# Kernel tuning notes

Measured on AMD Instinct MI355X. Metric: run time of the kernel, lower is better.

The kernel has to match this reference:

```python
import jax, jax.numpy as jnp
import numpy as np

T = 2048
HIDDEN = 4096
NH = 32        # query heads
NKV = 8        # kv heads
G = NH // NKV  # GQA group size
D = 128        # head_dim (== v_head_dim)
ROPE_BASE = 1000000.0


def setup_inputs() -> dict:
    key = jax.random.key(0)
    ks = jax.random.split(key, 8)
    s = 0.02
    return {
        "positions": jnp.arange(T, dtype=jnp.int32),
        "hidden_states": jax.random.normal(ks[0], (T, HIDDEN), dtype=jnp.float32),
        "Wq": jax.random.normal(ks[1], (HIDDEN, NH * D), dtype=jnp.float32) * s,
        "bq": jnp.zeros((NH * D,), dtype=jnp.float32),
        "Wk": jax.random.normal(ks[2], (HIDDEN, NKV * D), dtype=jnp.float32) * s,
        "bk": jnp.zeros((NKV * D,), dtype=jnp.float32),
        "Wv": jax.random.normal(ks[3], (HIDDEN, NKV * D), dtype=jnp.float32) * s,
        "bv": jnp.zeros((NKV * D,), dtype=jnp.float32),
        "Wo": jax.random.normal(ks[4], (NH * D, HIDDEN), dtype=jnp.float32) * s,
    }


def _rope(positions, x):
    # neox-style rotary, full rotary_dim = D
    half = D // 2
    inv_freq = 1.0 / (ROPE_BASE ** (jnp.arange(0, half, dtype=jnp.float32) / half))
    freqs = positions.astype(jnp.float32)[:, None] * inv_freq[None, :]  # [T, half]
    cos = jnp.cos(freqs)[:, None, :]  # [T, 1, half]
    sin = jnp.sin(freqs)[:, None, :]
    x1, x2 = x[..., :half], x[..., half:]
    return jnp.concatenate([x1 * cos - x2 * sin, x2 * cos + x1 * sin], axis=-1)


def reference(positions, hidden_states, Wq, bq, Wk, bk, Wv, bv, Wo):
    q = (hidden_states @ Wq + bq).reshape(T, NH, D)
    k = (hidden_states @ Wk + bk).reshape(T, NKV, D)
    v = (hidden_states @ Wv + bv).reshape(T, NKV, D)
    q = _rope(positions, q)
    k = _rope(positions, k)

    scale = D ** -0.5
    qg = q.reshape(T, NKV, G, D)
    # scores: [NKV, G, T(query), S(key)]
    scores = jnp.einsum("tkgd,skd->kgts", qg, k) * scale
    causal = positions[:, None] >= positions[None, :]  # [T, S]
    scores = jnp.where(causal[None, None, :, :], scores, jnp.finfo(scores.dtype).min)
    probs = jax.nn.softmax(scores, axis=-1)
    attn = jnp.einsum("kgts,skd->tkgd", probs, v).reshape(T, NH * D)

    output = attn @ Wo
    kv_fused = jnp.stack([k, v], axis=0)  # [2, T, NKV, D]
    return output, kv_fused
```

## Files before the change

### kernel.cpp

```cpp
#include <hip/hip_runtime.h>
#include <stdint.h>

#define T_SEQ 2048
#define HIDDEN_DIM 4096
#define NH 32
#define NKV 8
#define HD 128
#define QKV_N 6144

typedef unsigned short u16;
typedef __attribute__((__ext_vector_type__(8))) __bf16 bf16x8;
typedef __attribute__((__ext_vector_type__(4))) float f32x4;

__device__ __forceinline__ u16 f2bf(float f) {
    union { float f; unsigned u; } x; x.f = f;
    unsigned u = x.u;
    unsigned r = u + 0x7FFFu + ((u >> 16) & 1u);
    return (u16)(r >> 16);
}
__device__ __forceinline__ float bf2f(u16 h) {
    union { unsigned u; float f; } x; x.u = ((unsigned)h) << 16;
    return x.f;
}

__device__ __forceinline__ void gl_lds16(const u16* g, u16* l) {
    __builtin_amdgcn_global_load_lds((__attribute__((address_space(1))) void*)g,
                                     (__attribute__((address_space(3))) void*)l,
                                     16, 0, 0);
}

__global__ __launch_bounds__(256) void cast_f32_bf16(const float* __restrict__ in,
                                                     u16* __restrict__ out, int n4) {
    int i = blockIdx.x * 256 + threadIdx.x;
    if (i < n4) {
        float4 v = ((const float4*)in)[i];
        uint2 o;
        o.x = (unsigned)f2bf(v.x) | ((unsigned)f2bf(v.y) << 16);
        o.y = (unsigned)f2bf(v.z) | ((unsigned)f2bf(v.w) << 16);
        ((uint2*)out)[i] = o;
    }
}

__global__ __launch_bounds__(256) void transpose_cast(const float* __restrict__ W,
                                                      u16* __restrict__ Wt, int R, int C) {
    __shared__ float tile[32][33];
    int c0 = blockIdx.x * 32, r0 = blockIdx.y * 32;
    int tx = threadIdx.x & 31;
    int ty = threadIdx.x >> 5;
#pragma unroll
    for (int i = 0; i < 32; i += 8)
        tile[ty + i][tx] = W[(size_t)(r0 + ty + i) * C + c0 + tx];
    __syncthreads();
#pragma unroll
    for (int i = 0; i < 32; i += 8)
        Wt[(size_t)(c0 + ty + i) * R + r0 + tx] = f2bf(tile[tx][ty + i]);
}

__global__ __launch_bounds__(256) void concat_bias(const float* __restrict__ bq,
                                                   const float* __restrict__ bk,
                                                   const float* __restrict__ bv,
                                                   float* __restrict__ out) {
    int i = blockIdx.x * 256 + threadIdx.x;
    if (i < 4096) out[i] = bq[i];
    else if (i < 5120) out[i] = bk[i - 4096];
    else if (i < 6144) out[i] = bv[i - 5120];
}

template <int BF16_OUT, int HAS_BIAS>
__global__ __launch_bounds__(256) void gemm_bt(const u16* __restrict__ A,
                                               const u16* __restrict__ Bt,
                                               const float* __restrict__ bias,
                                               void* __restrict__ Cv,
                                               int M, int N, int K) {
    __shared__ alignas(16) u16 As[128 * 32];
    __shared__ alignas(16) u16 Bs[128 * 32];
    const int tid = threadIdx.x;
    const int wave = tid >> 6;
    const int lane = tid & 63;
    const int l15 = lane & 15;
    const int quad = lane >> 4;
    const int m0 = blockIdx.y * 128;
    const int n0 = blockIdx.x * 128;
    const int wm = (wave >> 1) * 64;
    const int wn = (wave & 1) * 64;

    f32x4 acc[4][4] = {};

    const u16* Ag = A + (size_t)(m0 + wave * 32 + (lane >> 2)) * K + (lane & 3) * 8;
    const u16* Bg = Bt + (size_t)(n0 + wave * 32 + (lane >> 2)) * K + (lane & 3) * 8;
    u16* Al = &As[wave * 32 * 32];
    u16* Bl = &Bs[wave * 32 * 32];

    for (int k0 = 0; k0 < K; k0 += 32) {
        __syncthreads();
        gl_lds16(Ag + k0, Al);
        gl_lds16(Ag + k0 + (size_t)16 * K, Al + 16 * 32);
        gl_lds16(Bg + k0, Bl);
        gl_lds16(Bg + k0 + (size_t)16 * K, Bl + 16 * 32);
        __syncthreads();
        bf16x8 af[4], bfr[4];
#pragma unroll
        for (int i = 0; i < 4; ++i)
            af[i] = *(const bf16x8*)&As[(wm + i * 16 + l15) * 32 + quad * 8];
#pragma unroll
        for (int i = 0; i < 4; ++i)
            bfr[i] = *(const bf16x8*)&Bs[(wn + i * 16 + l15) * 32 + quad * 8];
#pragma unroll
        for (int i = 0; i < 4; ++i)
#pragma unroll
            for (int j = 0; j < 4; ++j)
                acc[i][j] = __builtin_amdgcn_mfma_f32_16x16x32_bf16(af[i], bfr[j], acc[i][j], 0, 0, 0);
    }

#pragma unroll
    for (int i = 0; i < 4; ++i)
#pragma unroll
        for (int j = 0; j < 4; ++j)
#pragma unroll
            for (int r = 0; r < 4; ++r) {
                int row = m0 + wm + i * 16 + quad * 4 + r;
                int col = n0 + wn + j * 16 + l15;
                float v = acc[i][j][r];
                if (HAS_BIAS) v += bias[col];
                if (BF16_OUT) ((u16*)Cv)[(size_t)row * N + col] = f2bf(v);
                else ((float*)Cv)[(size_t)row * N + col] = v;
            }
}

__global__ __launch_bounds__(256) void rope_kernel(const int* __restrict__ positions,
                                                   const u16* __restrict__ qkv,
                                                   u16* __restrict__ qh,
                                                   u16* __restrict__ kh,
                                                   u16* __restrict__ vt,
                                                   float* __restrict__ kv_out) {
    const int t = blockIdx.x;
    const float pos = (float)positions[t];
    const size_t rowbase = (size_t)t * QKV_N;
    const float nlog = -13.815510557964274f / 64.f;
    for (int col = threadIdx.x; col < QKV_N; col += 256) {
        if (col < 4096) {
            int hh = col >> 7, d = col & 127, j = d & 63;
            float ang = pos * __expf((float)j * nlog);
            float cs = cosf(ang), sn = sinf(ang);
            size_t base = rowbase + (size_t)(col & ~127);
            float x1 = bf2f(qkv[base + j]);
            float x2 = bf2f(qkv[base + 64 + j]);
            float v = (d < 64) ? (x1 * cs - x2 * sn) : (x2 * cs + x1 * sn);
            qh[((size_t)hh * T_SEQ + t) * HD + d] = f2bf(v);
        } else if (col < 5120) {
            int lc = col - 4096, hh = lc >> 7, d = lc & 127, j = d & 63;
            float ang = pos * __expf((float)j * nlog);
            float cs = cosf(ang), sn = sinf(ang);
            size_t base = rowbase + 4096 + (size_t)hh * 128;
            float x1 = bf2f(qkv[base + j]);
            float x2 = bf2f(qkv[base + 64 + j]);
            float v = (d < 64) ? (x1 * cs - x2 * sn) : (x2 * cs + x1 * sn);
            kh[((size_t)hh * T_SEQ + t) * HD + d] = f2bf(v);
            kv_out[((size_t)t * NKV + hh) * HD + d] = v;
        } else {
            int lc = col - 5120, hh = lc >> 7, d = lc & 127;
            float v = bf2f(qkv[rowbase + 5120 + (size_t)hh * 128 + d]);
            vt[((size_t)hh * HD + d) * T_SEQ + t] = f2bf(v);
            kv_out[(((size_t)T_SEQ + t) * NKV + hh) * HD + d] = v;
        }
    }
}

#define KS_STRIDE 136
#define VS_STRIDE 72
#define PS_STRIDE 72

__global__ __launch_bounds__(256) void attn_kernel(const u16* __restrict__ Qh,
                                                   const u16* __restrict__ Kh,
                                                   const u16* __restrict__ Vt,
                                                   u16* __restrict__ attn_out) {
    __shared__ alignas(16) u16 Ks[64 * KS_STRIDE];
    __shared__ alignas(16) u16 Vs[128 * VS_STRIDE];
    __shared__ alignas(16) u16 Ps[4][32 * PS_STRIDE];

    const int h = blockIdx.y;
    const int qb = (gridDim.x - 1) - blockIdx.x;
    const int tid = threadIdx.x;
    const int wave = tid >> 6;
    const int lane = tid & 63;
    const int l15 = lane & 15;
    const int quad = lane >> 4;
    const int kvh = h >> 2;
    const int wrow0 = qb * 128 + wave * 32;

    const u16* Qp = Qh + ((size_t)h * T_SEQ + wrow0) * HD;
    const u16* Kp = Kh + (size_t)kvh * T_SEQ * HD;
    const u16* Vp = Vt + (size_t)kvh * HD * T_SEQ;

    bf16x8 aQ[2][4];
#pragma unroll
    for (int i = 0; i < 2; ++i)
#pragma unroll
        for (int kb = 0; kb < 4; ++kb)
            aQ[i][kb] = *(const bf16x8*)&Qp[(size_t)(i * 16 + l15) * HD + kb * 32 + quad * 8];

    f32x4 acc[2][8] = {};
    float mrow[2][4], lrow[2][4];
#pragma unroll
    for (int i = 0; i < 2; ++i)
#pragma unroll
        for (int r = 0; r < 4; ++r) { mrow[i][r] = -1e30f; lrow[i][r] = 0.f; }

    const float scale = 0.08838834764831845f;
    const int s_hi = qb * 128 + 128;

    const int krow = tid >> 4;
    const int kcol = (tid & 15) * 8;
    const int vrow = tid >> 3;
    const int vcol = (tid & 7) * 8;

    for (int s0 = 0; s0 < s_hi; s0 += 64) {
        __syncthreads();
#pragma unroll
        for (int rep = 0; rep < 4; ++rep) {
            int r = krow + rep * 16;
            *(uint4*)&Ks[r * KS_STRIDE + kcol] =
                *(const uint4*)&Kp[(size_t)(s0 + r) * HD + kcol];
        }
#pragma unroll
        for (int rep = 0; rep < 4; ++rep) {
            int d = vrow + rep * 32;
            *(uint4*)&Vs[d * VS_STRIDE + vcol] =
                *(const uint4*)&Vp[(size_t)d * T_SEQ + s0 + vcol];
        }
        __syncthreads();

        if (s0 <= wrow0 + 31) {
            f32x4 sc[2][4];
#pragma unroll
            for (int j = 0; j < 4; ++j) {
                f32x4 sa = {}, sb = {};
#pragma unroll
                for (int kb = 0; kb < 4; ++kb) {
                    bf16x8 bK = *(const bf16x8*)&Ks[(j * 16 + l15) * KS_STRIDE + kb * 32 + quad * 8];
                    sa = __builtin_amdgcn_mfma_f32_16x16x32_bf16(aQ[0][kb], bK, sa, 0, 0, 0);
                    sb = __builtin_amdgcn_mfma_f32_16x16x32_bf16(aQ[1][kb], bK, sb, 0, 0, 0);
                }
                sc[0][j] = sa;
                sc[1][j] = sb;
            }
#pragma unroll
            for (int i = 0; i < 2; ++i)
#pragma unroll
                for (int r = 0; r < 4; ++r) {
                    int t_idx = wrow0 + i * 16 + quad * 4 + r;
                    float pv[4];
                    float vmax = -1e30f;
#pragma unroll
                    for (int j = 0; j < 4; ++j) {
                        int s_idx = s0 + j * 16 + l15;
                        float v = sc[i][j][r] * scale;
                        v = (s_idx > t_idx) ? -1e30f : v;
                        pv[j] = v;
                        vmax = fmaxf(vmax, v);
                    }
#pragma unroll
                    for (int off = 1; off < 16; off <<= 1)
                        vmax = fmaxf(vmax, __shfl_xor(vmax, off));
                    float mn = fmaxf(mrow[i][r], vmax);
                    float alpha = __expf(mrow[i][r] - mn);
                    mrow[i][r] = mn;
                    float rs = 0.f;
#pragma unroll
                    for (int j = 0; j < 4; ++j) {
                        pv[j] = __expf(pv[j] - mn);
                        rs += pv[j];
                    }
#pragma unroll
                    for (int off = 1; off < 16; off <<= 1)
                        rs += __shfl_xor(rs, off);
                    lrow[i][r] = lrow[i][r] * alpha + rs;
#pragma unroll
                    for (int o = 0; o < 8; ++o)
                        acc[i][o][r] *= alpha;
#pragma unroll
                    for (int j = 0; j < 4; ++j)
                        Ps[wave][(i * 16 + quad * 4 + r) * PS_STRIDE + j * 16 + l15] = f2bf(pv[j]);
                }
            bf16x8 aP[2][2];
#pragma unroll
            for (int i = 0; i < 2; ++i)
#pragma unroll
                for (int k2 = 0; k2 < 2; ++k2)
                    aP[i][k2] = *(const bf16x8*)&Ps[wave][(i * 16 + l15) * PS_STRIDE + k2 * 32 + quad * 8];
#pragma unroll
            for (int o = 0; o < 8; ++o) {
                bf16x8 bV0 = *(const bf16x8*)&Vs[(o * 16 + l15) * VS_STRIDE + quad * 8];
                bf16x8 bV1 = *(const bf16x8*)&Vs[(o * 16 + l15) * VS_STRIDE + 32 + quad * 8];
#pragma unroll
                for (int i = 0; i < 2; ++i) {
                    acc[i][o] = __builtin_amdgcn_mfma_f32_16x16x32_bf16(aP[i][0], bV0, acc[i][o], 0, 0, 0);
                    acc[i][o] = __builtin_amdgcn_mfma_f32_16x16x32_bf16(aP[i][1], bV1, acc[i][o], 0, 0, 0);
                }
            }
        }
    }

#pragma unroll
    for (int i = 0; i < 2; ++i)
#pragma unroll
        for (int r = 0; r < 4; ++r) {
            float inv = 1.f / lrow[i][r];
            int t_idx = wrow0 + i * 16 + quad * 4 + r;
#pragma unroll
            for (int o = 0; o < 8; ++o)
                attn_out[(size_t)t_idx * (NH * HD) + h * HD + o * 16 + l15] =
                    f2bf(acc[i][o][r] * inv);
        }
}

extern "C" void kernel_launch(void* const* d_in, const int* in_sizes, int n_in,
                              void* d_out, int out_size, void* d_ws, size_t ws_size,
                              hipStream_t stream) {
    const int* positions = (const int*)d_in[0];
    const float* hidden = (const float*)d_in[1];
    const float* Wq = (const float*)d_in[2];
    const float* bq = (const float*)d_in[3];
    const float* Wk = (const float*)d_in[4];
    const float* bk = (const float*)d_in[5];
    const float* Wv = (const float*)d_in[6];
    const float* bv = (const float*)d_in[7];
    const float* Wo = (const float*)d_in[8];

    char* ws = (char*)d_ws;
    u16* hs_bf   = (u16*)(ws + 0);
    u16* attnbuf = (u16*)(ws + 0);
    u16* wqkvT   = (u16*)(ws + 16777216);
    u16* woT     = (u16*)(ws + 16777216);
    u16* qkvbuf  = (u16*)(ws + 67108864);
    u16* qbuf    = (u16*)(ws + 92274688);
    u16* kbuf    = (u16*)(ws + 109051904);
    u16* vtbuf   = (u16*)(ws + 113246208);
    float* biasb = (float*)(ws + 117440512);

    float* out0 = (float*)d_out;
    float* kvout = out0 + (size_t)T_SEQ * HIDDEN_DIM;

    cast_f32_bf16<<<dim3((T_SEQ * HIDDEN_DIM / 4 + 255) / 256), dim3(256), 0, stream>>>(
        hidden, hs_bf, T_SEQ * HIDDEN_DIM / 4);
    transpose_cast<<<dim3(128, 128), dim3(256), 0, stream>>>(Wq, wqkvT, HIDDEN_DIM, 4096);
    transpose_cast<<<dim3(32, 128), dim3(256), 0, stream>>>(Wk, wqkvT + (size_t)4096 * HIDDEN_DIM, HIDDEN_DIM, 1024);
    transpose_cast<<<dim3(32, 128), dim3(256), 0, stream>>>(Wv, wqkvT + (size_t)5120 * HIDDEN_DIM, HIDDEN_DIM, 1024);
    concat_bias<<<dim3(24), dim3(256), 0, stream>>>(bq, bk, bv, biasb);

    gemm_bt<1, 1><<<dim3(QKV_N / 128, T_SEQ / 128), dim3(256), 0, stream>>>(
        hs_bf, wqkvT, biasb, qkvbuf, T_SEQ, QKV_N, HIDDEN_DIM);

    transpose_cast<<<dim3(128, 128), dim3(256), 0, stream>>>(Wo, woT, NH * HD, HIDDEN_DIM);

    rope_kernel<<<dim3(T_SEQ), dim3(256), 0, stream>>>(positions, qkvbuf, qbuf, kbuf, vtbuf, kvout);

    attn_kernel<<<dim3(T_SEQ / 128, NH), dim3(256), 0, stream>>>(qbuf, kbuf, vtbuf, attnbuf);

    gemm_bt<0, 0><<<dim3(HIDDEN_DIM / 128, T_SEQ / 128), dim3(256), 0, stream>>>(
        attnbuf, woT, nullptr, out0, T_SEQ, HIDDEN_DIM, NH * HD);
}
```

Before: 646.1 us.

## Pair causal query blocks per workgroup, prefetch KV tiles, fold row-sum into MFMA

The attention grid is halved so each workgroup handles query block i and 15-i, which balances causal work across workgroups. K/V tiles for the next step are loaded into registers while the current tile is computed, so global latency overlaps with compute. The softmax row sum comes from an extra ones row appended to the V tile and accumulated by the MFMA, which removes the shuffle reductions, and exp is replaced by exp2 with the log2e factor folded into the scale. The cost is more registers, one extra MFMA column per step, and half as many workgroups.

```diff
diff --git a/kernel.cpp b/kernel.cpp
--- a/kernel.cpp
+++ b/kernel.cpp
@@ -11,6 +11,10 @@
 typedef unsigned short u16;
 typedef __attribute__((__ext_vector_type__(8))) __bf16 bf16x8;
 typedef __attribute__((__ext_vector_type__(4))) float f32x4;
+
+__device__ __forceinline__ float exp2_fast(float x) {
+    return __builtin_amdgcn_exp2f(x);
+}
 
 __device__ __forceinline__ u16 f2bf(float f) {
     union { float f; unsigned u; } x; x.f = f;
@@ -175,143 +179,172 @@
                                                    const u16* __restrict__ Vt,
                                                    u16* __restrict__ attn_out) {
     __shared__ alignas(16) u16 Ks[64 * KS_STRIDE];
-    __shared__ alignas(16) u16 Vs[128 * VS_STRIDE];
+    __shared__ alignas(16) u16 Vs[144 * VS_STRIDE];
     __shared__ alignas(16) u16 Ps[4][32 * PS_STRIDE];
 
     const int h = blockIdx.y;
-    const int qb = (gridDim.x - 1) - blockIdx.x;
     const int tid = threadIdx.x;
     const int wave = tid >> 6;
     const int lane = tid & 63;
     const int l15 = lane & 15;
     const int quad = lane >> 4;
     const int kvh = h >> 2;
-    const int wrow0 = qb * 128 + wave * 32;
-
-    const u16* Qp = Qh + ((size_t)h * T_SEQ + wrow0) * HD;
+
     const u16* Kp = Kh + (size_t)kvh * T_SEQ * HD;
     const u16* Vp = Vt + (size_t)kvh * HD * T_SEQ;
-
-    bf16x8 aQ[2][4];
-#pragma unroll
-    for (int i = 0; i < 2; ++i)
-#pragma unroll
-        for (int kb = 0; kb < 4; ++kb)
-            aQ[i][kb] = *(const bf16x8*)&Qp[(size_t)(i * 16 + l15) * HD + kb * 32 + quad * 8];
-
-    f32x4 acc[2][8] = {};
-    float mrow[2][4], lrow[2][4];
-#pragma unroll
-    for (int i = 0; i < 2; ++i)
-#pragma unroll
-        for (int r = 0; r < 4; ++r) { mrow[i][r] = -1e30f; lrow[i][r] = 0.f; }
-
-    const float scale = 0.08838834764831845f;
-    const int s_hi = qb * 128 + 128;
 
     const int krow = tid >> 4;
     const int kcol = (tid & 15) * 8;
     const int vrow = tid >> 3;
     const int vcol = (tid & 7) * 8;
 
-    for (int s0 = 0; s0 < s_hi; s0 += 64) {
-        __syncthreads();
-#pragma unroll
-        for (int rep = 0; rep < 4; ++rep) {
-            int r = krow + rep * 16;
-            *(uint4*)&Ks[r * KS_STRIDE + kcol] =
-                *(const uint4*)&Kp[(size_t)(s0 + r) * HD + kcol];
+    if (tid < 8) {
+        uint4 ones; ones.x = ones.y = ones.z = ones.w = 0x3F803F80u;
+        *(uint4*)&Vs[128 * VS_STRIDE + tid * 8] = ones;
+    } else if (tid < 128) {
+        int r = 129 + (tid - 8) / 8;
+        if (r < 144) {
+            uint4 z; z.x = z.y = z.z = z.w = 0u;
+            *(uint4*)&Vs[r * VS_STRIDE + (tid & 7) * 8] = z;
         }
-#pragma unroll
-        for (int rep = 0; rep < 4; ++rep) {
-            int d = vrow + rep * 32;
-            *(uint4*)&Vs[d * VS_STRIDE + vcol] =
-                *(const uint4*)&Vp[(size_t)d * T_SEQ + s0 + vcol];
+    }
+
+    const float kz = 0.08838834764831845f * 1.4426950408889634f;
+
+#pragma unroll 1
+    for (int pi = 0; pi < 2; ++pi) {
+        const int qb = pi ? (15 - blockIdx.x) : blockIdx.x;
+        const int wrow0 = qb * 128 + wave * 32;
+        const u16* Qp = Qh + ((size_t)h * T_SEQ + wrow0) * HD;
+
+        bf16x8 aQ[2][4];
+#pragma unroll
+        for (int i = 0; i < 2; ++i)
+#pragma unroll
+            for (int kb = 0; kb < 4; ++kb)
+                aQ[i][kb] = *(const bf16x8*)&Qp[(size_t)(i * 16 + l15) * HD + kb * 32 + quad * 8];
+
+        f32x4 acc[2][9];
+        float mrow[2][4];
+#pragma unroll
+        for (int i = 0; i < 2; ++i) {
+#pragma unroll
+            for (int o = 0; o < 9; ++o) acc[i][o] = (f32x4){0.f, 0.f, 0.f, 0.f};
+#pragma unroll
+            for (int r = 0; r < 4; ++r) mrow[i][r] = -1e30f;
         }
-        __syncthreads();
-
-        if (s0 <= wrow0 + 31) {
-            f32x4 sc[2][4];
-#pragma unroll
-            for (int j = 0; j < 4; ++j) {
-                f32x4 sa = {}, sb = {};
-#pragma unroll
-                for (int kb = 0; kb < 4; ++kb) {
-                    bf16x8 bK = *(const bf16x8*)&Ks[(j * 16 + l15) * KS_STRIDE + kb * 32 + quad * 8];
-                    sa = __builtin_amdgcn_mfma_f32_16x16x32_bf16(aQ[0][kb], bK, sa, 0, 0, 0);
-                    sb = __builtin_amdgcn_mfma_f32_16x16x32_bf16(aQ[1][kb], bK, sb, 0, 0, 0);
+
+        const int n_tiles = 2 * qb + 2;
+
+        uint4 kpre[4], vpre[4];
+#pragma unroll
+        for (int rep = 0; rep < 4; ++rep)
+            kpre[rep] = *(const uint4*)&Kp[(size_t)(krow + rep * 16) * HD + kcol];
+#pragma unroll
+        for (int rep = 0; rep < 4; ++rep)
+            vpre[rep] = *(const uint4*)&Vp[(size_t)(vrow + rep * 32) * T_SEQ + vcol];
+
+#pragma unroll 1
+        for (int t = 0; t < n_tiles; ++t) {
+            const int s0 = t * 64;
+            __syncthreads();
+#pragma unroll
+            for (int rep = 0; rep < 4; ++rep)
+                *(uint4*)&Ks[(krow + rep * 16) * KS_STRIDE + kcol] = kpre[rep];
+#pragma unroll
+            for (int rep = 0; rep < 4; ++rep)
+                *(uint4*)&Vs[(vrow + rep * 32) * VS_STRIDE + vcol] = vpre[rep];
+            __syncthreads();
+
+            if (t + 1 < n_tiles) {
+                const int sn = s0 + 64;
+#pragma unroll
+                for (int rep = 0; rep < 4; ++rep)
+                    kpre[rep] = *(const uint4*)&Kp[(size_t)(sn + krow + rep * 16) * HD + kcol];
+#pragma unroll
+                for (int rep = 0; rep < 4; ++rep)
+                    vpre[rep] = *(const uint4*)&Vp[(size_t)(vrow + rep * 32) * T_SEQ + sn + vcol];
+            }
+
+            if (s0 <= wrow0 + 31) {
+                f32x4 sc[2][4];
+#pragma unroll
+                for (int j = 0; j < 4; ++j) {
+                    f32x4 sa = {}, sb = {};
+#pragma unroll
+                    for (int kb = 0; kb < 4; ++kb) {
+                        bf16x8 bK = *(const bf16x8*)&Ks[(j * 16 + l15) * KS_STRIDE + kb * 32 + quad * 8];
+                        sa = __builtin_amdgcn_mfma_f32_16x16x32_bf16(aQ[0][kb], bK, sa, 0, 0, 0);
+                        sb = __builtin_amdgcn_mfma_f32_16x16x32_bf16(aQ[1][kb], bK, sb, 0, 0, 0);
+                    }
+                    sc[0][j] = sa;
+                    sc[1][j] = sb;
                 }
-                sc[0][j] = sa;
-                sc[1][j] = sb;
-            }
-#pragma unroll
-            for (int i = 0; i < 2; ++i)
-#pragma unroll
-                for (int r = 0; r < 4; ++r) {
-                    int t_idx = wrow0 + i * 16 + quad * 4 + r;
-                    float pv[4];
-                    float vmax = -1e30f;
-#pragma unroll
-                    for (int j = 0; j < 4; ++j) {
-                        int s_idx = s0 + j * 16 + l15;
-                        float v = sc[i][j][r] * scale;
-                        v = (s_idx > t_idx) ? -1e30f : v;
-                        pv[j] = v;
-                        vmax = fmaxf(vmax, v);
+#pragma unroll
+                for (int i = 0; i < 2; ++i) {
+                    float alpha4[4];
+#pragma unroll
+                    for (int r = 0; r < 4; ++r) {
+                        int t_idx = wrow0 + i * 16 + quad * 4 + r;
+                        float z[4];
+                        float vmax = -1e30f;
+#pragma unroll
+                        for (int j = 0; j < 4; ++j) {
+                            int s_idx = s0 + j * 16 + l15;
+                            float v = sc[i][j][r] * kz;
+                            v = (s_idx > t_idx) ? -1e30f : v;
+                            z[j] = v;
+                            vmax = fmaxf(vmax, v);
+                        }
+#pragma unroll
+                        for (int off = 1; off < 16; off <<= 1)
+                            vmax = fmaxf(vmax, __shfl_xor(vmax, off));
+                        float mn = fmaxf(mrow[i][r], vmax);
+                        alpha4[r] = exp2_fast(mrow[i][r] - mn);
+                        mrow[i][r] = mn;
+#pragma unroll
+                        for (int j = 0; j < 4; ++j) {
+                            float p = exp2_fast(z[j] - mn);
+                            Ps[wave][(i * 16 + quad * 4 + r) * PS_STRIDE + j * 16 + l15] = f2bf(p);
+                        }
                     }
-#pragma unroll
-                    for (int off = 1; off < 16; off <<= 1)
-                        vmax = fmaxf(vmax, __shfl_xor(vmax, off));
-                    float mn = fmaxf(mrow[i][r], vmax);
-                    float alpha = __expf(mrow[i][r] - mn);
-                    mrow[i][r] = mn;
-                    float rs = 0.f;
-#pragma unroll
-                    for (int j = 0; j < 4; ++j) {
-                        pv[j] = __expf(pv[j] - mn);
-                        rs += pv[j];
+                    f32x4 av = {alpha4[0], alpha4[1], alpha4[2], alpha4[3]};
+#pragma unroll
+                    for (int o = 0; o < 9; ++o)
+                        acc[i][o] *= av;
+                }
+                bf16x8 aP[2][2];
+#pragma unroll
+                for (int i = 0; i < 2; ++i)
+#pragma unroll
+                    for (int k2 = 0; k2 < 2; ++k2)
+                        aP[i][k2] = *(const bf16x8*)&Ps[wave][(i * 16 + l15) * PS_STRIDE + k2 * 32 + quad * 8];
+#pragma unroll
+                for (int o = 0; o < 9; ++o) {
+                    bf16x8 bV0 = *(const bf16x8*)&Vs[(o * 16 + l15) * VS_STRIDE + quad * 8];
+                    bf16x8 bV1 = *(const bf16x8*)&Vs[(o * 16 + l15) * VS_STRIDE + 32 + quad * 8];
+#pragma unroll
+                    for (int i = 0; i < 2; ++i) {
+                        acc[i][o] = __builtin_amdgcn_mfma_f32_16x16x32_bf16(aP[i][0], bV0, acc[i][o], 0, 0, 0);
+                        acc[i][o] = __builtin_amdgcn_mfma_f32_16x16x32_bf16(aP[i][1], bV1, acc[i][o], 0, 0, 0);
                     }
-#pragma unroll
-                    for (int off = 1; off < 16; off <<= 1)
-                        rs += __shfl_xor(rs, off);
-                    lrow[i][r] = lrow[i][r] * alpha + rs;
-#pragma unroll
-                    for (int o = 0; o < 8; ++o)
-                        acc[i][o][r] *= alpha;
-#pragma unroll
-                    for (int j = 0; j < 4; ++j)
-                        Ps[wave][(i * 16 + quad * 4 + r) * PS_STRIDE + j * 16 + l15] = f2bf(pv[j]);
-                }
-            bf16x8 aP[2][2];
-#pragma unroll
-            for (int i = 0; i < 2; ++i)
-#pragma unroll
-                for (int k2 = 0; k2 < 2; ++k2)
-                    aP[i][k2] = *(const bf16x8*)&Ps[wave][(i * 16 + l15) * PS_STRIDE + k2 * 32 + quad * 8];
-#pragma unroll
-            for (int o = 0; o < 8; ++o) {
-                bf16x8 bV0 = *(const bf16x8*)&Vs[(o * 16 + l15) * VS_STRIDE + quad * 8];
-                bf16x8 bV1 = *(const bf16x8*)&Vs[(o * 16 + l15) * VS_STRIDE + 32 + quad * 8];
-#pragma unroll
-                for (int i = 0; i < 2; ++i) {
-                    acc[i][o] = __builtin_amdgcn_mfma_f32_16x16x32_bf16(aP[i][0], bV0, acc[i][o], 0, 0, 0);
-                    acc[i][o] = __builtin_amdgcn_mfma_f32_16x16x32_bf16(aP[i][1], bV1, acc[i][o], 0, 0, 0);
                 }
             }
         }
-    }
-
-#pragma unroll
-    for (int i = 0; i < 2; ++i)
-#pragma unroll
-        for (int r = 0; r < 4; ++r) {
-            float inv = 1.f / lrow[i][r];
-            int t_idx = wrow0 + i * 16 + quad * 4 + r;
-#pragma unroll
-            for (int o = 0; o < 8; ++o)
-                attn_out[(size_t)t_idx * (NH * HD) + h * HD + o * 16 + l15] =
-                    f2bf(acc[i][o][r] * inv);
-        }
+
+#pragma unroll
+        for (int i = 0; i < 2; ++i)
+#pragma unroll
+            for (int r = 0; r < 4; ++r) {
+                float l = __shfl(acc[i][8][r], lane & 48);
+                float inv = 1.f / l;
+                int t_idx = wrow0 + i * 16 + quad * 4 + r;
+#pragma unroll
+                for (int o = 0; o < 8; ++o)
+                    attn_out[(size_t)t_idx * (NH * HD) + h * HD + o * 16 + l15] =
+                        f2bf(acc[i][o][r] * inv);
+            }
+    }
 }
 
 extern "C" void kernel_launch(void* const* d_in, const int* in_sizes, int n_in,
@@ -355,7 +388,7 @@
 
     rope_kernel<<<dim3(T_SEQ), dim3(256), 0, stream>>>(positions, qkvbuf, qbuf, kbuf, vtbuf, kvout);
 
-    attn_kernel<<<dim3(T_SEQ / 128, NH), dim3(256), 0, stream>>>(qbuf, kbuf, vtbuf, attnbuf);
+    attn_kernel<<<dim3(8, NH), dim3(256), 0, stream>>>(qbuf, kbuf, vtbuf, attnbuf);
 
     gemm_bt<0, 0><<<dim3(HIDDEN_DIM / 128, T_SEQ / 128), dim3(256), 0, stream>>>(
         attnbuf, woT, nullptr, out0, T_SEQ, HIDDEN_DIM, NH * HD);
```

After: 699.9 us. 8.3% more time.
